# Optimization experiments

Measured on AMD Instinct MI355X. Metric: run time of the kernel, lower is better.

The kernel has to match this reference:

```python
import jax, jax.numpy as jnp
import numpy as np

N, IN_DIM, HID, M, T, E, A, OUT = 10000, 256, 256, 8, 3, 160000, 2000, 10
LN_EPS = 1e-5


def _layernorm(x, g, b):
    mu = x.mean(-1, keepdims=True)
    var = ((x - mu) ** 2).mean(-1, keepdims=True)
    return (x - mu) * jax.lax.rsqrt(var + LN_EPS) * g + b


def _gcn_conv(x, w, b, src, dst, n):
    # PyG GCNConv: x' = D^{-1/2}(A+I)D^{-1/2} (x W) + b, deg counted on dst with self-loops
    xw = x @ w  # [n, out]
    loops = jnp.arange(n, dtype=src.dtype)
    s = jnp.concatenate([src, loops])
    d = jnp.concatenate([dst, loops])
    deg = jax.ops.segment_sum(jnp.ones(d.shape[0], xw.dtype), d, num_segments=n)
    dinv = jax.lax.rsqrt(jnp.maximum(deg, 1.0))
    norm = dinv[s] * dinv[d]
    out = jax.ops.segment_sum(xw[s] * norm[:, None], d, num_segments=n)
    return out + b


def setup_inputs() -> dict:
    key = jax.random.key(0)
    ks = jax.random.split(key, 26)
    g = lambda i, shape: (jax.random.normal(ks[i], shape, jnp.float32) * 0.02)
    return {
        "edge_index_t": jax.random.randint(ks[0], (T, 2, E), 0, N),
        "node_t": jax.random.randint(ks[1], (T, A), 0, N),
        "m": M,
        "emb": g(2, (N, IN_DIM)),
        "gcn_w1": g(3, (IN_DIM, HID)), "gcn_b1": jnp.zeros((HID,), jnp.float32),
        "gcn_w2": g(4, (HID, HID)), "gcn_b2": jnp.zeros((HID,), jnp.float32),
        "ln1_g": jnp.ones((HID,), jnp.float32), "ln1_b": jnp.zeros((HID,), jnp.float32),
        "tok_w1": g(5, (M, M)), "tok_b1": jnp.zeros((M,), jnp.float32),
        "tok_w2": g(6, (M, M)), "tok_b2": jnp.zeros((M,), jnp.float32),
        "ln2_g": jnp.ones((HID,), jnp.float32), "ln2_b": jnp.zeros((HID,), jnp.float32),
        "ch_w1": g(7, (HID, HID)), "ch_b1": jnp.zeros((HID,), jnp.float32),
        "ch_w2": g(8, (HID, HID)), "ch_b2": jnp.zeros((HID,), jnp.float32),
        "pred_w": g(9, (HID, HID)), "pred_b": jnp.zeros((HID,), jnp.float32),
        "cls1_w": g(10, (HID, HID)), "cls1_b": jnp.zeros((HID,), jnp.float32),
        "cls2_w": g(11, (HID, OUT)), "cls2_b": jnp.zeros((OUT,), jnp.float32),
    }


def reference(edge_index_t, node_t, m, emb,
              gcn_w1, gcn_b1, gcn_w2, gcn_b2,
              ln1_g, ln1_b, tok_w1, tok_b1, tok_w2, tok_b2,
              ln2_g, ln2_b, ch_w1, ch_b1, ch_w2, ch_b2,
              pred_w, pred_b, cls1_w, cls1_b, cls2_w, cls2_b):
    n = emb.shape[0]

    def mixer(xm):  # [n, m, hid]
        y = _layernorm(xm, ln1_g, ln1_b)
        # token MLP over the m axis (transpose(1,2) in torch)
        y = jnp.einsum('nmh,mk->nkh', y, tok_w1) + tok_b1[None, :, None]
        y = jax.nn.gelu(y, approximate=False)
        y = jnp.einsum('nmh,mk->nkh', y, tok_w2) + tok_b2[None, :, None]
        x = xm + y
        z = _layernorm(x, ln2_g, ln2_b)
        z = jax.nn.gelu(z @ ch_w1 + ch_b1, approximate=False) @ ch_w2 + ch_b2
        return x + z

    def step(x_m, inp):
        src, dst, nid = inp
        # forecast from current window (before this step's graph update)
        x_new = mixer(x_m).mean(axis=1)  # discrete FinalProcessLayer: mean over tokens
        # 2-layer GCN on the (shared) initial embeddings
        x = _gcn_conv(emb, gcn_w1, gcn_b1, src, dst, n)
        x = jax.nn.relu(x)
        x = _gcn_conv(x, gcn_w2, gcn_b2, src, dst, n)
        # boolean-mask scatter: zero rows of nodes listed in node_t[i]
        x = x.at[nid].set(0.0)
        x_m = jnp.concatenate([x_m[:, 1:, :], x[:, None, :]], axis=1)
        return x_m, x_new

    x_m0 = jnp.zeros((n, m, HID), emb.dtype)
    _, v = jax.lax.scan(step, x_m0, (edge_index_t[:, 0], edge_index_t[:, 1], node_t))
    # InvariantPredictor over all T timesteps at once: v [T, n, hid]
    h = jnp.tanh(v @ pred_w + pred_b)
    y_hat = jax.nn.relu((h @ cls1_w + cls1_b) @ cls2_w + cls2_b)
    return h, y_hat
```

## Files before the change

kernel.cpp:

```cpp
#include <hip/hip_runtime.h>
#include <math.h>

#define NN 10000
#define HIDD 256
#define MTOK 8
#define TT 3
#define EE 160000
#define AA 2000
#define OUTD 10
#define LNEPS 1e-5f

typedef unsigned short u16;
typedef __attribute__((ext_vector_type(8))) __bf16 bf16x8;
typedef __attribute__((ext_vector_type(4))) float f32x4;

__device__ __forceinline__ float gelu_f(float x) {
    return 0.5f * x * (1.f + erff(x * 0.7071067811865475f));
}
__device__ __forceinline__ u16 f2bf(float x) {
    unsigned u = __builtin_bit_cast(unsigned, x);
    return (u16)((u + 0x7FFFu + ((u >> 16) & 1u)) >> 16);
}
__device__ __forceinline__ float bf2f(u16 b) {
    return __builtin_bit_cast(float, (unsigned)b << 16);
}
__device__ __forceinline__ void gload16(const void* g, void* l) {
    __builtin_amdgcn_global_load_lds(
        (const __attribute__((address_space(1))) unsigned int*)g,
        (__attribute__((address_space(3))) unsigned int*)l, 16, 0, 0);
}

__global__ void count_kernel(const int* __restrict__ edge, int* __restrict__ cnt) {
    int g = blockIdx.y;
    const int* dst = edge + (size_t)g * 2 * EE + EE;
    int e = blockIdx.x * 256 + threadIdx.x;
    if (e < EE) atomicAdd(&cnt[g * NN + dst[e]], 1);
}

__global__ __launch_bounds__(1024) void scan_kernel(const int* __restrict__ cnt_all,
        int* __restrict__ rowstart_all, int* __restrict__ cursor_all, float* __restrict__ dinv_all) {
    int g = blockIdx.x;
    const int* cnt = cnt_all + (size_t)g * NN;
    int* rowstart = rowstart_all + (size_t)g * NN;
    int* cursor = cursor_all + (size_t)g * NN;
    float* dinv = dinv_all + (size_t)g * NN;
    __shared__ int wsum[16];
    int tid = threadIdx.x, lane = tid & 63, wid = tid >> 6;
    int carry = 0;
    for (int base = 0; base < NN; base += 1024) {
        int i = base + tid;
        int v = (i < NN) ? cnt[i] : 0;
        int s = v;
        #pragma unroll
        for (int o = 1; o < 64; o <<= 1) {
            int t = __shfl_up(s, o, 64);
            if (lane >= o) s += t;
        }
        if (lane == 63) wsum[wid] = s;
        __syncthreads();
        if (wid == 0) {
            int ws = (lane < 16) ? wsum[lane] : 0;
            #pragma unroll
            for (int o = 1; o < 16; o <<= 1) {
                int t = __shfl_up(ws, o, 64);
                if (lane >= o) ws += t;
            }
            if (lane < 16) wsum[lane] = ws;
        }
        __syncthreads();
        int woff = (wid > 0) ? wsum[wid - 1] : 0;
        int tot = wsum[15];
        if (i < NN) {
            int excl = carry + s + woff - v;
            rowstart[i] = excl;
            cursor[i] = excl;
            dinv[i] = rsqrtf((float)(v + 1));
        }
        carry += tot;
        __syncthreads();
    }
}

__global__ void fill_kernel(const int* __restrict__ edge, int* __restrict__ cursor, int* __restrict__ esrc) {
    int g = blockIdx.y;
    const int* src = edge + (size_t)g * 2 * EE;
    const int* dst = src + EE;
    int e = blockIdx.x * 256 + threadIdx.x;
    if (e < EE) {
        int d = dst[e];
        int idx = atomicAdd(&cursor[g * NN + d], 1);
        esrc[(size_t)g * EE + idx] = src[e];
    }
}

template<int RELU, int WF32, int WSPLIT>
__global__ __launch_bounds__(256) void gcn_agg(const float* __restrict__ xw, size_t xw_goff,
        const int* __restrict__ esrc_all, const int* __restrict__ rowstart_all,
        const int* __restrict__ cnt_all, const float* __restrict__ dinv_all,
        const float* __restrict__ bias, float* __restrict__ out,
        u16* __restrict__ ohi, u16* __restrict__ olo) {
    int g = blockIdx.y;
    const float* xwg = xw + (size_t)g * xw_goff;
    const int* esrc = esrc_all + (size_t)g * EE;
    const int* rowstart = rowstart_all + (size_t)g * NN;
    const int* cntp = cnt_all + (size_t)g * NN;
    const float* dinv = dinv_all + (size_t)g * NN;
    int wave = threadIdx.x >> 6, lane = threadIdx.x & 63;
    int d = blockIdx.x * 4 + wave;
    if (d >= NN) return;
    int start = rowstart[d];
    int len = cntp[d];
    float dd = dinv[d];
    int h = lane * 4;
    float4 a = *(const float4*)&xwg[(size_t)d * HIDD + h];
    float4 acc;
    acc.x = a.x * dd; acc.y = a.y * dd; acc.z = a.z * dd; acc.w = a.w * dd;
    for (int i = 0; i < len; i++) {
        int s = esrc[start + i];
        float ds = dinv[s];
        float4 b = *(const float4*)&xwg[(size_t)s * HIDD + h];
        acc.x = fmaf(b.x, ds, acc.x);
        acc.y = fmaf(b.y, ds, acc.y);
        acc.z = fmaf(b.z, ds, acc.z);
        acc.w = fmaf(b.w, ds, acc.w);
    }
    float o0 = acc.x * dd + bias[h + 0];
    float o1 = acc.y * dd + bias[h + 1];
    float o2 = acc.z * dd + bias[h + 2];
    float o3 = acc.w * dd + bias[h + 3];
    if (RELU) {
        o0 = fmaxf(o0, 0.f); o1 = fmaxf(o1, 0.f); o2 = fmaxf(o2, 0.f); o3 = fmaxf(o3, 0.f);
    }
    size_t obase = (size_t)g * NN * HIDD + (size_t)d * HIDD + h;
    if (WF32) {
        float4 o; o.x = o0; o.y = o1; o.z = o2; o.w = o3;
        *(float4*)&out[obase] = o;
    }
    if (WSPLIT) {
        ushort4 hv, lv;
        u16 h0 = f2bf(o0), h1 = f2bf(o1), h2 = f2bf(o2), h3 = f2bf(o3);
        hv.x = h0; hv.y = h1; hv.z = h2; hv.w = h3;
        lv.x = f2bf(o0 - bf2f(h0)); lv.y = f2bf(o1 - bf2f(h1));
        lv.z = f2bf(o2 - bf2f(h2)); lv.w = f2bf(o3 - bf2f(h3));
        *(ushort4*)&ohi[obase] = hv;
        *(ushort4*)&olo[obase] = lv;
    }
}

__global__ void mask_kernel(const int* __restrict__ node_t, float* __restrict__ xs) {
    int g = blockIdx.y;
    int node = node_t[(size_t)g * AA + blockIdx.x];
    xs[(size_t)g * NN * HIDD + (size_t)node * HIDD + threadIdx.x] = 0.f;
}

__global__ void split_kernel(const float* __restrict__ x, u16* __restrict__ hi, u16* __restrict__ lo, int n) {
    int i = blockIdx.x * 256 + threadIdx.x;
    if (i < n) {
        float v = x[i];
        u16 h = f2bf(v);
        hi[i] = h;
        lo[i] = f2bf(v - bf2f(h));
    }
}

__global__ void wsplit_all(const float* __restrict__ w0, const float* __restrict__ w1,
        const float* __restrict__ w2, const float* __restrict__ w3,
        const float* __restrict__ w4, const float* __restrict__ w5, u16* __restrict__ bt) {
    const float* W[6] = { w0, w1, w2, w3, w4, w5 };
    const float* Wm = W[blockIdx.y];
    u16* Bt = bt + (size_t)blockIdx.y * 256 * 768;
    int c = blockIdx.x, k = threadIdx.x;
    float x = Wm[k * 256 + c];
    u16 hi = f2bf(x), lo = f2bf(x - bf2f(hi));
    Bt[c * 768 + k] = hi;
    Bt[c * 768 + 256 + k] = hi;
    Bt[c * 768 + 512 + k] = lo;
}

template<int ACT, int WF32, int WSPLIT, int EPI>
__global__ __launch_bounds__(256) void gemm_split(
        const u16* __restrict__ Ahi, const u16* __restrict__ Alo,
        const u16* __restrict__ Bt, const float* __restrict__ bias,
        float* __restrict__ outf, u16* __restrict__ ohi, u16* __restrict__ olo,
        const float* __restrict__ xsum, int R) {
    __shared__ __align__(16) u16 ldsA[3][128 * 64];
    __shared__ __align__(16) u16 ldsB[2][128 * 64];
    int tid = threadIdx.x;
    int lane = tid & 63, w = tid >> 6;
    int nwg = gridDim.x, orig = blockIdx.x;
    int xcd = orig & 7, i8 = orig >> 3;
    int q = nwg >> 3, r = nwg & 7;
    int bid = (xcd < r ? xcd * (q + 1) : r * (q + 1) + (xcd - r) * q) + i8;
    int rowbase = (bid >> 1) * 128;
    int cb = bid & 1;
    int wrow = (w >> 1) * 64, wcol = (w & 1) * 64;
    f32x4 acc[4][4];
    #pragma unroll
    for (int i = 0; i < 4; i++)
        #pragma unroll
        for (int j = 0; j < 4; j++) acc[i][j] = f32x4{0.f, 0.f, 0.f, 0.f};

    constexpr int KCH[12]  = {0,4,1,5,2,6,3,7,8,9,10,11};
    constexpr int BNEW[12] = {1,0,1,0,1,0,1,0,1,1,1,1};
    constexpr int BBUF[12] = {0,0,1,1,0,0,1,1,0,1,0,1};
    constexpr int VMC[12]  = {8,12,8,12,8,12,8,12,12,12,8,0};

    auto stageA = [&](int slot, int c) {
        const u16* Aseg = (c >= 4 && c < 8) ? Alo : Ahi;
        int koff = (c & 3) * 64;
        #pragma unroll
        for (int i = 0; i < 4; i++) {
            int j = i * 256 + tid;
            int rr = j >> 3, sl = j & 7;
            int grow = rowbase + rr; if (grow > R - 1) grow = R - 1;
            const u16* gp = Aseg + (size_t)grow * 256 + koff + ((sl ^ (rr & 7)) << 3);
            gload16(gp, &ldsA[slot][(i * 256 + (tid & 192)) << 3]);
        }
    };
    auto stageB = [&](int buf, int c) {
        #pragma unroll
        for (int i = 0; i < 4; i++) {
            int j = i * 256 + tid;
            int rr = j >> 3, sl = j & 7;
            const u16* gp = Bt + (size_t)(cb * 128 + rr) * 768 + c * 64 + ((sl ^ (rr & 7)) << 3);
            gload16(gp, &ldsB[buf][(i * 256 + (tid & 192)) << 3]);
        }
    };

    stageB(0, KCH[0]);
    stageA(0, KCH[0]);
    stageA(1, KCH[1]);
    #pragma unroll
    for (int p = 0; p < 12; p++) {
        if (p + 1 <= 11 && BNEW[p + 1]) stageB(BBUF[p + 1], KCH[p + 1]);
        if (p + 2 <= 11) stageA((p + 2) % 3, KCH[p + 2]);
        if (VMC[p] == 12)      asm volatile("s_waitcnt vmcnt(12)" ::: "memory");
        else if (VMC[p] == 8)  asm volatile("s_waitcnt vmcnt(8)" ::: "memory");
        else                   asm volatile("s_waitcnt vmcnt(0)" ::: "memory");
        __builtin_amdgcn_s_barrier();
        __builtin_amdgcn_sched_barrier(0);
        __builtin_amdgcn_s_setprio(1);
        #pragma unroll
        for (int ks = 0; ks < 2; ks++) {
            bf16x8 a[4], b[4];
            #pragma unroll
            for (int rf = 0; rf < 4; rf++) {
                int rr = wrow + rf * 16 + (lane & 15);
                int slot = (lane >> 4) + ks * 4;
                a[rf] = *(const bf16x8*)&ldsA[p % 3][(rr << 6) + ((slot ^ (rr & 7)) << 3)];
            }
            #pragma unroll
            for (int cf = 0; cf < 4; cf++) {
                int cc = wcol + cf * 16 + (lane & 15);
                int slot = (lane >> 4) + ks * 4;
                b[cf] = *(const bf16x8*)&ldsB[BBUF[p]][(cc << 6) + ((slot ^ (cc & 7)) << 3)];
            }
            #pragma unroll
            for (int rf = 0; rf < 4; rf++)
                #pragma unroll
                for (int cf = 0; cf < 4; cf++)
                    acc[rf][cf] = __builtin_amdgcn_mfma_f32_16x16x32_bf16(a[rf], b[cf], acc[rf][cf], 0, 0, 0);
        }
        __builtin_amdgcn_s_setprio(0);
        __builtin_amdgcn_sched_barrier(0);
        __builtin_amdgcn_s_barrier();
    }
    #pragma unroll
    for (int rf = 0; rf < 4; rf++) {
        #pragma unroll
        for (int cf = 0; cf < 4; cf++) {
            int col = cb * 128 + wcol + cf * 16 + (lane & 15);
            float bv = bias[col];
            f32x4 v = acc[rf][cf];
            if (EPI == 1) {
                float s = 0.f;
                #pragma unroll
                for (int r2 = 0; r2 < 4; r2++) s += gelu_f(v[r2] + bv);
                float o = __shfl_xor(s, 16, 64);
                float nodesum = s + o;
                if (((lane >> 4) & 1) == 0) {
                    int node = ((rowbase + wrow + rf * 16) >> 3) + ((lane >> 4) >> 1);
                    u16 hi = f2bf(nodesum), lo = f2bf(nodesum - bf2f(hi));
                    ohi[(size_t)node * 256 + col] = hi;
                    olo[(size_t)node * 256 + col] = lo;
                }
            } else {
                int row0 = rowbase + wrow + rf * 16 + ((lane >> 4) << 2);
                #pragma unroll
                for (int r2 = 0; r2 < 4; r2++) {
                    int row = row0 + r2;
                    if (row < R) {
                        float val = v[r2] + bv;
                        if (ACT == 1) val = gelu_f(val);
                        if (ACT == 2) val = tanhf(val);
                        if (WF32) outf[(size_t)row * 256 + col] = val;
                        if (WSPLIT) {
                            u16 hi = f2bf(val), lo = f2bf(val - bf2f(hi));
                            ohi[(size_t)row * 256 + col] = hi;
                            olo[(size_t)row * 256 + col] = lo;
                        }
                    }
                }
            }
        }
    }
}

__global__ __launch_bounds__(512, 2) void tail_fused(
        const u16* __restrict__ s2_hi, const u16* __restrict__ s2_lo,
        const float* __restrict__ xsum,
        const u16* __restrict__ Bt_cw2, const float* __restrict__ cb2,
        const u16* __restrict__ Bt_pred, const float* __restrict__ pred_b,
        const u16* __restrict__ Bt_cls1, const float* __restrict__ cls1_b,
        const float* __restrict__ cls2_w, const float* __restrict__ cls2_b,
        float* __restrict__ h_out1, float* __restrict__ y_out1, int R) {
    __shared__ __align__(16) u16 ldsA[2][32 * 256];
    __shared__ __align__(16) u16 ldsB[256 * 64];
    int tid = threadIdx.x;
    int lane = tid & 63, wid = tid >> 6;
    int wrow = (wid & 1) * 16, wcol = (wid >> 1) * 64;
    int rowbase = blockIdx.x * 32;

    constexpr int KCH[12]  = {0,4,1,5,2,6,3,7,8,9,10,11};
    constexpr int BNEW[12] = {1,0,1,0,1,0,1,0,1,1,1,1};

    auto stageB = [&](int c, const u16* Bt) {
        #pragma unroll
        for (int i = 0; i < 4; i++) {
            int j = i * 512 + tid;
            int cc = j >> 3, sl = j & 7;
            const u16* gp = Bt + (size_t)cc * 768 + c * 64 + ((sl ^ (cc & 7)) << 3);
            gload16(gp, &ldsB[(i * 512 + (tid & 448)) << 3]);
        }
    };
    #pragma unroll
    for (int seg = 0; seg < 2; seg++) {
        const u16* src = seg ? s2_lo : s2_hi;
        #pragma unroll
        for (int i = 0; i < 2; i++) {
            int j = i * 512 + tid;
            int rr = j >> 5;
            int gch = (j >> 3) & 3, t = j & 7;
            int rowG = rowbase + rr; if (rowG > R - 1) rowG = R - 1;
            const u16* gp = src + (size_t)rowG * 256 + gch * 64 + ((t ^ (rr & 7)) << 3);
            gload16(gp, &ldsA[seg][(i * 512 + (tid & 448)) << 3]);
        }
    }

    for (int s = 0; s < 3; s++) {
        const u16* Bt = (s == 0) ? Bt_cw2 : (s == 1) ? Bt_pred : Bt_cls1;
        f32x4 acc[4];
        #pragma unroll
        for (int i = 0; i < 4; i++) acc[i] = f32x4{0.f, 0.f, 0.f, 0.f};
        #pragma unroll
        for (int p = 0; p < 12; p++) {
            if (BNEW[p]) {
                asm volatile("s_waitcnt lgkmcnt(0)" ::: "memory");
                __builtin_amdgcn_s_barrier();
                stageB(KCH[p], Bt);
                asm volatile("s_waitcnt vmcnt(0)" ::: "memory");
                __builtin_amdgcn_s_barrier();
            }
            __builtin_amdgcn_sched_barrier(0);
            __builtin_amdgcn_s_setprio(1);
            int c = KCH[p];
            int seg = (c >= 4 && c < 8) ? 1 : 0;
            int kbase = (c & 3) * 64;
            #pragma unroll
            for (int ks = 0; ks < 2; ks++) {
                int rr = wrow + (lane & 15);
                int slot = (lane >> 4) + ks * 4;
                bf16x8 a = *(const bf16x8*)&ldsA[seg][rr * 256 + kbase + ((slot ^ (rr & 7)) << 3)];
                #pragma unroll
                for (int cf = 0; cf < 4; cf++) {
                    int cc = wcol + cf * 16 + (lane & 15);
                    bf16x8 b = *(const bf16x8*)&ldsB[cc * 64 + ((slot ^ (cc & 7)) << 3)];
                    acc[cf] = __builtin_amdgcn_mfma_f32_16x16x32_bf16(a, b, acc[cf], 0, 0, 0);
                }
            }
            __builtin_amdgcn_s_setprio(0);
            __builtin_amdgcn_sched_barrier(0);
        }
        __builtin_amdgcn_s_barrier();
        #pragma unroll
        for (int cf = 0; cf < 4; cf++) {
            int col = wcol + cf * 16 + (lane & 15);
            #pragma unroll
            for (int r2 = 0; r2 < 4; r2++) {
                int row = wrow + ((lane >> 4) << 2) + r2;
                int rowG = rowbase + row;
                int rowC = rowG > R - 1 ? R - 1 : rowG;
                float av = acc[cf][r2];
                int pos = row * 256 + (col >> 6) * 64 + ((((col >> 3) & 7) ^ (row & 7)) << 3) + (col & 7);
                if (s == 0) {
                    float val = (xsum[(size_t)rowC * 256 + col] + av + 8.f * cb2[col]) * 0.125f;
                    u16 hi = f2bf(val), lo = f2bf(val - bf2f(hi));
                    ldsA[0][pos] = hi;
                    ldsA[1][pos] = lo;
                } else if (s == 1) {
                    float h = tanhf(av + pred_b[col]);
                    if (rowG < R) h_out1[(size_t)rowG * 256 + col] = h;
                    u16 hi = f2bf(h), lo = f2bf(h - bf2f(hi));
                    ldsA[0][pos] = hi;
                    ldsA[1][pos] = lo;
                } else {
                    ((float*)ldsA)[row * 256 + (col ^ (row & 31))] = av + cls1_b[col];
                }
            }
        }
    }
    float* w2 = (float*)ldsB;
    for (int i = tid; i < 256 * OUTD; i += 512) w2[i] = cls2_w[i];
    asm volatile("s_waitcnt lgkmcnt(0) vmcnt(0)" ::: "memory");
    __builtin_amdgcn_s_barrier();
    const float* gbuf = (const float*)ldsA;
    for (int o = tid; o < 32 * OUTD; o += 512) {
        int row = o / OUTD, j = o - row * OUTD;
        int rowG = rowbase + row;
        if (rowG < R) {
            float a2 = 0.f;
            for (int k = 0; k < 256; k++) a2 = fmaf(gbuf[row * 256 + (k ^ (row & 31))], w2[k * OUTD + j], a2);
            y_out1[(size_t)rowG * OUTD + j] = fmaxf(a2 + cls2_b[j], 0.f);
        }
    }
}

__global__ __launch_bounds__(256) void mixer_front(
        const float* __restrict__ xs, int nodebase,
        const float* __restrict__ ln1_g, const float* __restrict__ ln1_b,
        const float* __restrict__ tw1, const float* __restrict__ tb1,
        const float* __restrict__ tw2, const float* __restrict__ tb2,
        const float* __restrict__ ln2_g, const float* __restrict__ ln2_b,
        u16* __restrict__ z_hi, u16* __restrict__ z_lo, float* __restrict__ xsum_out) {
    int nv = nodebase + blockIdx.x;
    int step = nv >= NN ? 1 : 0;
    int n = nv - step * NN;
    const float* p1 = xs + ((size_t)step * NN + n) * HIDD;
    const float* p2 = step ? xs + (size_t)n * HIDD : nullptr;
    int tid = threadIdx.x;
    int wave = tid >> 6, lane = tid & 63;
    __shared__ __align__(16) float sx[MTOK][HIDD];
    __shared__ float stw1h[16], stw2[64], stb1[8], stb2[8], sw1s6[8];
    __shared__ float red[MTOK][2];
    if (tid < 16) stw1h[tid] = tw1[48 + tid];
    if (tid < 64) stw2[tid] = tw2[tid];
    if (tid < 8) {
        stb1[tid] = tb1[tid]; stb2[tid] = tb2[tid];
        float s = 0.f;
        #pragma unroll
        for (int m = 0; m < 6; m++) s += tw1[m * MTOK + tid];
        sw1s6[tid] = s;
    }
    sx[6][tid] = p2 ? p2[tid] : 0.f;
    sx[7][tid] = p1[tid];
    __syncthreads();
    float g1v = ln1_g[tid], b1v = ln1_b[tid];
    if (wave < 2) {
        int m = 6 + wave;
        float x0 = sx[m][lane], x1 = sx[m][lane + 64], x2 = sx[m][lane + 128], x3 = sx[m][lane + 192];
        float s = x0 + x1 + x2 + x3;
        float ss = x0 * x0 + x1 * x1 + x2 * x2 + x3 * x3;
        for (int off = 32; off > 0; off >>= 1) { s += __shfl_down(s, off, 64); ss += __shfl_down(ss, off, 64); }
        if (lane == 0) {
            float mu = s * (1.f / HIDD);
            float var = ss * (1.f / HIDD) - mu * mu;
            red[m][0] = mu;
            red[m][1] = rsqrtf(var + LNEPS);
        }
    }
    __syncthreads();
    float x6 = sx[6][tid], x7 = sx[7][tid];
    float ty6 = (x6 - red[6][0]) * red[6][1] * g1v + b1v;
    float ty7 = (x7 - red[7][0]) * red[7][1] * g1v + b1v;
    float u[MTOK];
    #pragma unroll
    for (int k = 0; k < MTOK; k++) {
        float a = stb1[k];
        a = fmaf(b1v, sw1s6[k], a);
        a = fmaf(ty6, stw1h[k], a);
        a = fmaf(ty7, stw1h[8 + k], a);
        u[k] = gelu_f(a);
    }
    float xsm = 0.f;
    #pragma unroll
    for (int k = 0; k < MTOK; k++) {
        float a = stb2[k];
        #pragma unroll
        for (int m = 0; m < MTOK; m++) a = fmaf(u[m], stw2[m * MTOK + k], a);
        if (k == 6) a += x6;
        if (k == 7) a += x7;
        sx[k][tid] = a;
        xsm += a;
    }
    xsum_out[(size_t)nv * HIDD + tid] = xsm;
    __syncthreads();
    float g2v = ln2_g[tid], b2v = ln2_b[tid];
    #pragma unroll
    for (int rep = 0; rep < 2; rep++) {
        int m = wave + rep * 4;
        float x0 = sx[m][lane], x1 = sx[m][lane + 64], x2 = sx[m][lane + 128], x3 = sx[m][lane + 192];
        float s = x0 + x1 + x2 + x3;
        float ss = x0 * x0 + x1 * x1 + x2 * x2 + x3 * x3;
        for (int off = 32; off > 0; off >>= 1) { s += __shfl_down(s, off, 64); ss += __shfl_down(ss, off, 64); }
        if (lane == 0) {
            float mu = s * (1.f / HIDD);
            float var = ss * (1.f / HIDD) - mu * mu;
            red[m][0] = mu;
            red[m][1] = rsqrtf(var + LNEPS);
        }
    }
    __syncthreads();
    #pragma unroll
    for (int m = 0; m < MTOK; m++) {
        float z = (sx[m][tid] - red[m][0]) * red[m][1] * g2v + b2v;
        u16 hi = f2bf(z), lo = f2bf(z - bf2f(hi));
        size_t idx = ((size_t)blockIdx.x * MTOK + m) * HIDD + tid;
        z_hi[idx] = hi;
        z_lo[idx] = lo;
    }
}

__global__ __launch_bounds__(256) void mixer_kernel(
        const float* __restrict__ ln1_g, const float* __restrict__ ln1_b,
        const float* __restrict__ tw1, const float* __restrict__ tb1,
        const float* __restrict__ tw2, const float* __restrict__ tb2,
        const float* __restrict__ ln2_g, const float* __restrict__ ln2_b,
        const float* __restrict__ cw1, const float* __restrict__ cb1,
        const float* __restrict__ cw2, const float* __restrict__ cb2,
        float* __restrict__ vout) {
    int tid = threadIdx.x;
    __shared__ __align__(16) float sx[MTOK][HIDD];
    __shared__ __align__(16) float sy[MTOK][HIDD];
    __shared__ float stw1[64], stw2[64], stb1[8], stb2[8];
    if (tid < 64) { stw1[tid] = tw1[tid]; stw2[tid] = tw2[tid]; }
    if (tid < 8)  { stb1[tid] = tb1[tid]; stb2[tid] = tb2[tid]; }
    __syncthreads();
    float b1v = ln1_b[tid];
    float ty[MTOK];
    #pragma unroll
    for (int m = 0; m < MTOK; m++) ty[m] = b1v;
    float u[MTOK];
    #pragma unroll
    for (int k = 0; k < MTOK; k++) {
        float a = stb1[k];
        #pragma unroll
        for (int m = 0; m < MTOK; m++) a = fmaf(ty[m], stw1[m * MTOK + k], a);
        u[k] = gelu_f(a);
    }
    #pragma unroll
    for (int k = 0; k < MTOK; k++) {
        float a = stb2[k];
        #pragma unroll
        for (int m = 0; m < MTOK; m++) a = fmaf(u[m], stw2[m * MTOK + k], a);
        sx[k][tid] = a;
    }
    __syncthreads();
    __shared__ float red[MTOK][2];
    int wave = tid >> 6, lane = tid & 63;
    float g2v = ln2_g[tid], b2v = ln2_b[tid];
    #pragma unroll
    for (int rep = 0; rep < 2; rep++) {
        int m = wave + rep * 4;
        float x0 = sx[m][lane], x1 = sx[m][lane + 64], x2 = sx[m][lane + 128], x3 = sx[m][lane + 192];
        float s = x0 + x1 + x2 + x3;
        float ss = x0 * x0 + x1 * x1 + x2 * x2 + x3 * x3;
        for (int off = 32; off > 0; off >>= 1) { s += __shfl_down(s, off, 64); ss += __shfl_down(ss, off, 64); }
        if (lane == 0) {
            float mu = s * (1.f / HIDD);
            float var = ss * (1.f / HIDD) - mu * mu;
            red[m][0] = mu;
            red[m][1] = rsqrtf(var + LNEPS);
        }
    }
    __syncthreads();
    #pragma unroll
    for (int m = 0; m < MTOK; m++) sy[m][tid] = (sx[m][tid] - red[m][0]) * red[m][1] * g2v + b2v;
    __syncthreads();
    float acc[MTOK];
    #pragma unroll
    for (int m = 0; m < MTOK; m++) acc[m] = 0.f;
    for (int h = 0; h < HIDD; h += 4) {
        float w0 = cw1[(h + 0) * HIDD + tid];
        float w1 = cw1[(h + 1) * HIDD + tid];
        float w2 = cw1[(h + 2) * HIDD + tid];
        float w3 = cw1[(h + 3) * HIDD + tid];
        #pragma unroll
        for (int m = 0; m < MTOK; m++) {
            const float4 a = *(const float4*)&sy[m][h];
            acc[m] = fmaf(a.x, w0, acc[m]);
            acc[m] = fmaf(a.y, w1, acc[m]);
            acc[m] = fmaf(a.z, w2, acc[m]);
            acc[m] = fmaf(a.w, w3, acc[m]);
        }
    }
    __syncthreads();
    float cb1v = cb1[tid];
    #pragma unroll
    for (int m = 0; m < MTOK; m++) sy[m][tid] = gelu_f(acc[m] + cb1v);
    __syncthreads();
    float acc2[MTOK];
    #pragma unroll
    for (int m = 0; m < MTOK; m++) acc2[m] = 0.f;
    for (int h = 0; h < HIDD; h += 4) {
        float w0 = cw2[(h + 0) * HIDD + tid];
        float w1 = cw2[(h + 1) * HIDD + tid];
        float w2 = cw2[(h + 2) * HIDD + tid];
        float w3 = cw2[(h + 3) * HIDD + tid];
        #pragma unroll
        for (int m = 0; m < MTOK; m++) {
            const float4 a = *(const float4*)&sy[m][h];
            acc2[m] = fmaf(a.x, w0, acc2[m]);
            acc2[m] = fmaf(a.y, w1, acc2[m]);
            acc2[m] = fmaf(a.z, w2, acc2[m]);
            acc2[m] = fmaf(a.w, w3, acc2[m]);
        }
    }
    float cb2v = cb2[tid];
    float ssum = 0.f;
    #pragma unroll
    for (int m = 0; m < MTOK; m++) ssum += sx[m][tid] + acc2[m] + cb2v;
    vout[tid] = ssum * (1.f / MTOK);
}

__global__ __launch_bounds__(256) void t0_head(const float* __restrict__ v0row,
        const float* __restrict__ pred_w, const float* __restrict__ pred_b,
        const float* __restrict__ cls1_w, const float* __restrict__ cls1_b,
        const float* __restrict__ cls2_w, const float* __restrict__ cls2_b,
        float* __restrict__ h0row, float* __restrict__ y0row) {
    __shared__ float s[HIDD], s2[HIDD];
    int tid = threadIdx.x;
    s[tid] = v0row[tid];
    __syncthreads();
    float a = 0.f;
    for (int k = 0; k < HIDD; k++) a = fmaf(s[k], pred_w[k * HIDD + tid], a);
    float h = tanhf(a + pred_b[tid]);
    h0row[tid] = h;
    s2[tid] = h;
    __syncthreads();
    a = 0.f;
    for (int k = 0; k < HIDD; k++) a = fmaf(s2[k], cls1_w[k * HIDD + tid], a);
    float g = a + cls1_b[tid];
    __syncthreads();
    s[tid] = g;
    __syncthreads();
    if (tid < OUTD) {
        float y = 0.f;
        for (int k = 0; k < HIDD; k++) y = fmaf(s[k], cls2_w[k * OUTD + tid], y);
        y0row[tid] = fmaxf(y + cls2_b[tid], 0.f);
    }
}

__global__ void bcast_both(const float* __restrict__ h0row, const float* __restrict__ y0row,
        float* __restrict__ hout, float* __restrict__ yout) {
    int n = blockIdx.x, tid = threadIdx.x;
    hout[(size_t)n * HIDD + tid] = h0row[tid];
    if (tid < OUTD) yout[(size_t)n * OUTD + tid] = y0row[tid];
}

extern "C" void kernel_launch(void* const* d_in, const int* in_sizes, int n_in,
                              void* d_out, int out_size, void* d_ws, size_t ws_size,
                              hipStream_t stream) {
    const int* edge    = (const int*)d_in[0];
    const int* node_t  = (const int*)d_in[1];
    const float* emb   = (const float*)d_in[3];
    const float* gcn_w1 = (const float*)d_in[4];
    const float* gcn_b1 = (const float*)d_in[5];
    const float* gcn_w2 = (const float*)d_in[6];
    const float* gcn_b2 = (const float*)d_in[7];
    const float* ln1_g = (const float*)d_in[8];
    const float* ln1_b = (const float*)d_in[9];
    const float* tw1   = (const float*)d_in[10];
    const float* tb1   = (const float*)d_in[11];
    const float* tw2   = (const float*)d_in[12];
    const float* tb2   = (const float*)d_in[13];
    const float* ln2_g = (const float*)d_in[14];
    const float* ln2_b = (const float*)d_in[15];
    const float* cw1   = (const float*)d_in[16];
    const float* cb1   = (const float*)d_in[17];
    const float* cw2   = (const float*)d_in[18];
    const float* cb2   = (const float*)d_in[19];
    const float* pred_w = (const float*)d_in[20];
    const float* pred_b = (const float*)d_in[21];
    const float* cls1_w = (const float*)d_in[22];
    const float* cls1_b = (const float*)d_in[23];
    const float* cls2_w = (const float*)d_in[24];
    const float* cls2_b = (const float*)d_in[25];

    const size_t NH = (size_t)NN * HIDD;
    char* wsb = (char*)d_ws;
    size_t off = 0;
    auto alloc = [&](size_t bytes) { char* p = wsb + off; off = (off + bytes + 255) & ~(size_t)255; return p; };
    float* xs   = (float*)alloc(2 * NH * 4);
    u16* v_hi   = (u16*)alloc(2 * NH * 2);
    u16* v_lo   = (u16*)alloc(2 * NH * 2);
    u16* h_hi   = (u16*)alloc(2 * NH * 2);
    u16* h_lo   = (u16*)alloc(2 * NH * 2);
    float* xw2  = (float*)alloc(2 * NH * 4);
    float* xsum = (float*)alloc(2 * NH * 4);
    u16* Bt_all = (u16*)alloc((size_t)6 * 256 * 768 * 2);
    u16* Bt_cw1  = Bt_all;
    u16* Bt_cw2  = Bt_all + 1 * 256 * 768;
    u16* Bt_pred = Bt_all + 2 * 256 * 768;
    u16* Bt_cls1 = Bt_all + 3 * 256 * 768;
    u16* Bt_gw1  = Bt_all + 4 * 256 * 768;
    u16* Bt_gw2  = Bt_all + 5 * 256 * 768;
    float* dinv  = (float*)alloc(2 * NN * 4);
    float* zeros = (float*)alloc(HIDD * 4);
    float* v0row = (float*)alloc(HIDD * 4);
    float* h0row = (float*)alloc(HIDD * 4);
    float* y0row = (float*)alloc(16 * 4);
    int* cnt    = (int*)alloc(2 * NN * 4);
    int* rowst  = (int*)alloc(2 * NN * 4);
    int* cursor = (int*)alloc(2 * NN * 4);
    int* esrc   = (int*)alloc((size_t)2 * EE * 4);
    float* xw    = (float*)h_hi;
    u16*  emb_hi = h_lo;
    u16*  emb_lo = h_lo + NH;
    u16*  agg_hi = v_hi;
    u16*  agg_lo = v_lo;
    u16*  s2_hi  = (u16*)xw2;
    u16*  s2_lo  = (u16*)xw2 + 2 * NH;
    size_t remain = (ws_size > off + 4096) ? (ws_size - off - 4096) : 0;
    int CHN = (int)(remain / 8192);
    if (CHN > 2 * NN) CHN = 2 * NN;
    CHN &= ~15;
    if (CHN < 16) CHN = 16;
    const size_t ZE = (size_t)CHN * MTOK * HIDD;
    u16* z_hi  = (u16*)alloc(ZE * 2);
    u16* z_lo  = (u16*)alloc(ZE * 2);

    float* h_out = (float*)d_out;
    float* y_out = h_out + (size_t)TT * NH;

    hipMemsetAsync(zeros, 0, HIDD * sizeof(float), stream);
    wsplit_all<<<dim3(256, 6), 256, 0, stream>>>(cw1, cw2, pred_w, cls1_w, gcn_w1, gcn_w2, Bt_all);
    split_kernel<<<(NN * HIDD + 255) / 256, 256, 0, stream>>>(emb, emb_hi, emb_lo, NN * HIDD);
    gemm_split<0, 1, 0, 0><<<2 * ((NN + 127) / 128), 256, 0, stream>>>(
        emb_hi, emb_lo, Bt_gw1, zeros, xw, nullptr, nullptr, nullptr, NN);

    mixer_kernel<<<1, 256, 0, stream>>>(ln1_g, ln1_b, tw1, tb1, tw2, tb2,
        ln2_g, ln2_b, cw1, cb1, cw2, cb2, v0row);
    t0_head<<<1, 256, 0, stream>>>(v0row, pred_w, pred_b, cls1_w, cls1_b,
        cls2_w, cls2_b, h0row, y0row);
    bcast_both<<<NN, 256, 0, stream>>>(h0row, y0row, h_out, y_out);

    hipMemsetAsync(cnt, 0, 2 * NN * sizeof(int), stream);
    count_kernel<<<dim3((EE + 255) / 256, 2), 256, 0, stream>>>(edge, cnt);
    scan_kernel<<<2, 1024, 0, stream>>>(cnt, rowst, cursor, dinv);
    fill_kernel<<<dim3((EE + 255) / 256, 2), 256, 0, stream>>>(edge, cursor, esrc);
    gcn_agg<1, 0, 1><<<dim3((NN + 3) / 4, 2), 256, 0, stream>>>(xw, 0,
        esrc, rowst, cnt, dinv, gcn_b1, nullptr, agg_hi, agg_lo);
    gemm_split<0, 1, 0, 0><<<2 * ((2 * NN + 127) / 128), 256, 0, stream>>>(
        agg_hi, agg_lo, Bt_gw2, zeros, xw2, nullptr, nullptr, nullptr, 2 * NN);
    gcn_agg<0, 1, 0><<<dim3((NN + 3) / 4, 2), 256, 0, stream>>>(xw2, NH,
        esrc, rowst, cnt, dinv, gcn_b2, xs, nullptr, nullptr);
    mask_kernel<<<dim3(AA, 2), 256, 0, stream>>>(node_t, xs);

    for (int nb = 0; nb < 2 * NN; nb += CHN) {
        int nodes = 2 * NN - nb < CHN ? 2 * NN - nb : CHN;
        int R = nodes * MTOK;
        int rb = (R + 127) / 128;
        mixer_front<<<nodes, 256, 0, stream>>>(xs, nb,
            ln1_g, ln1_b, tw1, tb1, tw2, tb2, ln2_g, ln2_b, z_hi, z_lo, xsum);
        gemm_split<1, 0, 0, 1><<<2 * rb, 256, 0, stream>>>(
            z_hi, z_lo, Bt_cw1, cb1, nullptr,
            s2_hi + (size_t)nb * HIDD, s2_lo + (size_t)nb * HIDD, nullptr, R);
    }
    tail_fused<<<(2 * NN + 31) / 32, 512, 0, stream>>>(
        s2_hi, s2_lo, xsum,
        Bt_cw2, cb2, Bt_pred, pred_b, Bt_cls1, cls1_b, cls2_w, cls2_b,
        h_out + NH, y_out + (size_t)NN * OUTD, 2 * NN);
}
```

Before: 518.8 us.

## Restructure split-bf16 GEMM pipeline per K-chunk and dual-accumulate GCN gather

The split-precision GEMM now walks four K chunks. Each chunk loads the A-hi and A-lo tiles together and reuses one B-hi tile for both MFMAs, then runs a second pass of A-hi against a B-lo tile that is prefetched during the first pass. This replaces the 12-step interleaved schedule and its three-slot A ring. The goal is fewer B-tile loads and barriers per chunk, but waits now sit at coarser boundaries and the first pass has less latency hiding. The GCN aggregation loop is also unrolled by two with a second accumulator, so two neighbor-row gathers can be in flight at once.

```diff
diff --git a/kernel.cpp b/kernel.cpp
--- a/kernel.cpp
+++ b/kernel.cpp
@@ -113,17 +113,32 @@
     float dd = dinv[d];
     int h = lane * 4;
     float4 a = *(const float4*)&xwg[(size_t)d * HIDD + h];
-    float4 acc;
+    float4 acc, accB;
     acc.x = a.x * dd; acc.y = a.y * dd; acc.z = a.z * dd; acc.w = a.w * dd;
-    for (int i = 0; i < len; i++) {
-        int s = esrc[start + i];
-        float ds = dinv[s];
-        float4 b = *(const float4*)&xwg[(size_t)s * HIDD + h];
-        acc.x = fmaf(b.x, ds, acc.x);
-        acc.y = fmaf(b.y, ds, acc.y);
-        acc.z = fmaf(b.z, ds, acc.z);
-        acc.w = fmaf(b.w, ds, acc.w);
-    }
+    accB.x = 0.f; accB.y = 0.f; accB.z = 0.f; accB.w = 0.f;
+    int i = 0;
+    for (; i + 2 <= len; i += 2) {
+        int s0 = esrc[start + i];
+        int s1 = esrc[start + i + 1];
+        float d0 = dinv[s0];
+        float d1 = dinv[s1];
+        float4 b0 = *(const float4*)&xwg[(size_t)s0 * HIDD + h];
+        float4 b1 = *(const float4*)&xwg[(size_t)s1 * HIDD + h];
+        acc.x = fmaf(b0.x, d0, acc.x);  accB.x = fmaf(b1.x, d1, accB.x);
+        acc.y = fmaf(b0.y, d0, acc.y);  accB.y = fmaf(b1.y, d1, accB.y);
+        acc.z = fmaf(b0.z, d0, acc.z);  accB.z = fmaf(b1.z, d1, accB.z);
+        acc.w = fmaf(b0.w, d0, acc.w);  accB.w = fmaf(b1.w, d1, accB.w);
+    }
+    if (i < len) {
+        int s0 = esrc[start + i];
+        float d0 = dinv[s0];
+        float4 b0 = *(const float4*)&xwg[(size_t)s0 * HIDD + h];
+        acc.x = fmaf(b0.x, d0, acc.x);
+        acc.y = fmaf(b0.y, d0, acc.y);
+        acc.z = fmaf(b0.z, d0, acc.z);
+        acc.w = fmaf(b0.w, d0, acc.w);
+    }
+    acc.x += accB.x; acc.y += accB.y; acc.z += accB.z; acc.w += accB.w;
     float o0 = acc.x * dd + bias[h + 0];
     float o1 = acc.y * dd + bias[h + 1];
     float o2 = acc.z * dd + bias[h + 2];
@@ -183,7 +198,8 @@
         const u16* __restrict__ Bt, const float* __restrict__ bias,
         float* __restrict__ outf, u16* __restrict__ ohi, u16* __restrict__ olo,
         const float* __restrict__ xsum, int R) {
-    __shared__ __align__(16) u16 ldsA[3][128 * 64];
+    __shared__ __align__(16) u16 ldsAhi[2][128 * 64];
+    __shared__ __align__(16) u16 ldsAlo[128 * 64];
     __shared__ __align__(16) u16 ldsB[2][128 * 64];
     int tid = threadIdx.x;
     int lane = tid & 63, w = tid >> 6;
@@ -200,21 +216,26 @@
         #pragma unroll
         for (int j = 0; j < 4; j++) acc[i][j] = f32x4{0.f, 0.f, 0.f, 0.f};
 
-    constexpr int KCH[12]  = {0,4,1,5,2,6,3,7,8,9,10,11};
-    constexpr int BNEW[12] = {1,0,1,0,1,0,1,0,1,1,1,1};
-    constexpr int BBUF[12] = {0,0,1,1,0,0,1,1,0,1,0,1};
-    constexpr int VMC[12]  = {8,12,8,12,8,12,8,12,12,12,8,0};
-
-    auto stageA = [&](int slot, int c) {
-        const u16* Aseg = (c >= 4 && c < 8) ? Alo : Ahi;
-        int koff = (c & 3) * 64;
+    auto stageAhi = [&](int slot, int k) {
+        int koff = k * 64;
         #pragma unroll
         for (int i = 0; i < 4; i++) {
             int j = i * 256 + tid;
             int rr = j >> 3, sl = j & 7;
             int grow = rowbase + rr; if (grow > R - 1) grow = R - 1;
-            const u16* gp = Aseg + (size_t)grow * 256 + koff + ((sl ^ (rr & 7)) << 3);
-            gload16(gp, &ldsA[slot][(i * 256 + (tid & 192)) << 3]);
+            const u16* gp = Ahi + (size_t)grow * 256 + koff + ((sl ^ (rr & 7)) << 3);
+            gload16(gp, &ldsAhi[slot][(i * 256 + (tid & 192)) << 3]);
+        }
+    };
+    auto stageAlo = [&](int k) {
+        int koff = k * 64;
+        #pragma unroll
+        for (int i = 0; i < 4; i++) {
+            int j = i * 256 + tid;
+            int rr = j >> 3, sl = j & 7;
+            int grow = rowbase + rr; if (grow > R - 1) grow = R - 1;
+            const u16* gp = Alo + (size_t)grow * 256 + koff + ((sl ^ (rr & 7)) << 3);
+            gload16(gp, &ldsAlo[(i * 256 + (tid & 192)) << 3]);
         }
     };
     auto stageB = [&](int buf, int c) {
@@ -227,16 +248,53 @@
         }
     };
 
-    stageB(0, KCH[0]);
-    stageA(0, KCH[0]);
-    stageA(1, KCH[1]);
-    #pragma unroll
-    for (int p = 0; p < 12; p++) {
-        if (p + 1 <= 11 && BNEW[p + 1]) stageB(BBUF[p + 1], KCH[p + 1]);
-        if (p + 2 <= 11) stageA((p + 2) % 3, KCH[p + 2]);
-        if (VMC[p] == 12)      asm volatile("s_waitcnt vmcnt(12)" ::: "memory");
-        else if (VMC[p] == 8)  asm volatile("s_waitcnt vmcnt(8)" ::: "memory");
-        else                   asm volatile("s_waitcnt vmcnt(0)" ::: "memory");
+    stageAhi(0, 0);
+    stageAlo(0);
+    stageB(0, 0);
+    #pragma unroll
+    for (int k = 0; k < 4; k++) {
+        int sh = k & 1;
+        stageB(1, 8 + k);
+        asm volatile("s_waitcnt vmcnt(4)" ::: "memory");
+        __builtin_amdgcn_s_barrier();
+        __builtin_amdgcn_sched_barrier(0);
+        __builtin_amdgcn_s_setprio(1);
+        #pragma unroll
+        for (int ks = 0; ks < 2; ks++) {
+            bf16x8 ah[4], al[4], b[4];
+            #pragma unroll
+            for (int rf = 0; rf < 4; rf++) {
+                int rr = wrow + rf * 16 + (lane & 15);
+                int slot = (lane >> 4) + ks * 4;
+                int offi = (rr << 6) + ((slot ^ (rr & 7)) << 3);
+                ah[rf] = *(const bf16x8*)&ldsAhi[sh][offi];
+                al[rf] = *(const bf16x8*)&ldsAlo[offi];
+            }
+            #pragma unroll
+            for (int cf = 0; cf < 4; cf++) {
+                int cc = wcol + cf * 16 + (lane & 15);
+                int slot = (lane >> 4) + ks * 4;
+                b[cf] = *(const bf16x8*)&ldsB[0][(cc << 6) + ((slot ^ (cc & 7)) << 3)];
+            }
+            #pragma unroll
+            for (int rf = 0; rf < 4; rf++)
+                #pragma unroll
+                for (int cf = 0; cf < 4; cf++) {
+                    acc[rf][cf] = __builtin_amdgcn_mfma_f32_16x16x32_bf16(ah[rf], b[cf], acc[rf][cf], 0, 0, 0);
+                    acc[rf][cf] = __builtin_amdgcn_mfma_f32_16x16x32_bf16(al[rf], b[cf], acc[rf][cf], 0, 0, 0);
+                }
+        }
+        __builtin_amdgcn_s_setprio(0);
+        __builtin_amdgcn_sched_barrier(0);
+        __builtin_amdgcn_s_barrier();
+        if (k < 3) {
+            stageAhi(sh ^ 1, k + 1);
+            stageAlo(k + 1);
+            stageB(0, k + 1);
+            asm volatile("s_waitcnt vmcnt(12)" ::: "memory");
+        } else {
+            asm volatile("s_waitcnt vmcnt(0)" ::: "memory");
+        }
         __builtin_amdgcn_s_barrier();
         __builtin_amdgcn_sched_barrier(0);
         __builtin_amdgcn_s_setprio(1);
@@ -247,13 +305,13 @@
             for (int rf = 0; rf < 4; rf++) {
                 int rr = wrow + rf * 16 + (lane & 15);
                 int slot = (lane >> 4) + ks * 4;
-                a[rf] = *(const bf16x8*)&ldsA[p % 3][(rr << 6) + ((slot ^ (rr & 7)) << 3)];
+                a[rf] = *(const bf16x8*)&ldsAhi[sh][(rr << 6) + ((slot ^ (rr & 7)) << 3)];
             }
             #pragma unroll
             for (int cf = 0; cf < 4; cf++) {
                 int cc = wcol + cf * 16 + (lane & 15);
                 int slot = (lane >> 4) + ks * 4;
-                b[cf] = *(const bf16x8*)&ldsB[BBUF[p]][(cc << 6) + ((slot ^ (cc & 7)) << 3)];
+                b[cf] = *(const bf16x8*)&ldsB[1][(cc << 6) + ((slot ^ (cc & 7)) << 3)];
             }
             #pragma unroll
             for (int rf = 0; rf < 4; rf++)
```

After: 499.3 us. 3.8% less time.
